# Performance work log

Hardware: AMD Instinct MI355X
Metric: run time of the kernel (lower is better)

Reference implementation:

```python
import jax, jax.numpy as jnp
import numpy as np

NUM_HEADS = 16


def setup_inputs() -> dict:
    key = jax.random.key(0)
    ks = jax.random.split(key, 7)
    B, N, D = 16, 512, 1024
    return {
        "x": jax.random.normal(ks[0], (B, N, D), dtype=jnp.float32),
        "spatial_encoding": jax.random.normal(ks[1], (B, N, N), dtype=jnp.float32),
        "edge_encoding": jax.random.normal(ks[2], (B, N, N), dtype=jnp.float32),
        "Wq": jax.random.normal(ks[3], (D, D), dtype=jnp.float32) * (D ** -0.5),
        "Wk": jax.random.normal(ks[4], (D, D), dtype=jnp.float32) * (D ** -0.5),
        "Wv": jax.random.normal(ks[5], (D, D), dtype=jnp.float32) * (D ** -0.5),
        "Wo": jax.random.normal(ks[6], (D, D), dtype=jnp.float32) * (D ** -0.5),
    }


def reference(x, spatial_encoding, edge_encoding, Wq, Wk, Wv, Wo):
    B, N, D = x.shape
    H = NUM_HEADS
    hd = D // H
    scale = D ** -0.5  # NOTE: source scales by hidden_dim**-0.5, not head_size**-0.5

    def split_heads(t):  # (B,N,D) -> (B,H,N,hd)
        return t.reshape(B, N, H, hd).transpose(0, 2, 1, 3)

    q = split_heads(x @ Wq.T)
    k = split_heads(x @ Wk.T)
    v = split_heads(x @ Wv.T)

    bias = (spatial_encoding + edge_encoding)[:, None]  # (B,1,N,N)
    a = jnp.einsum("bhnd,bhmd->bhnm", q, k) * scale + bias  # (B,H,N,N)

    # rows that are entirely zero (padded) are masked to -inf
    row_nonzero = jnp.any(a != 0, axis=-1, keepdims=True)  # (B,H,N,1)
    a = jnp.where(row_nonzero, a, -jnp.inf)
    p = jax.nn.softmax(a, axis=-1)
    p = jnp.where(jnp.isnan(p), 0.0, p)  # nan_to_num after softmax of all -inf rows

    o = jnp.einsum("bhnm,bhmd->bhnd", p, v)  # (B,H,N,hd)
    o = o.transpose(0, 2, 1, 3).reshape(B, N, D)
    return o @ Wo.T
```

## Files before the change

kernel.cpp:

```cpp
#include <hip/hip_runtime.h>
#include <cstdint>


typedef unsigned short u16;
typedef unsigned int   u32;
typedef __attribute__((ext_vector_type(8))) short bf8;
typedef __attribute__((ext_vector_type(4))) float f4;

__device__ __forceinline__ u16 f2bf(float x) {
  u32 u = __float_as_uint(x);
  u += 0x7FFF + ((u >> 16) & 1);
  return (u16)(u >> 16);
}

__device__ __forceinline__ float bf2f(u16 x) {
  return __uint_as_float(((u32)x) << 16);
}

__device__ __forceinline__ void gl2lds16(const void* g, void* l) {
  __builtin_amdgcn_global_load_lds(
      (const __attribute__((address_space(1))) u32*)g,
      (__attribute__((address_space(3))) u32*)l, 16, 0, 0);
}

__device__ __forceinline__ void barrier_raw() {
  asm volatile("" ::: "memory");
  __builtin_amdgcn_s_barrier();
  asm volatile("" ::: "memory");
}


__global__ __launch_bounds__(256) void cast_bf16(const float* __restrict__ src,
                                                 uint4* __restrict__ dst, int n8) {
  const int i = blockIdx.x * 256 + threadIdx.x;
  if (i >= n8) return;
  const float4* s = (const float4*)src;
  const float4 a = s[2 * i], c = s[2 * i + 1];
  uint4 o;
  o.x = (u32)f2bf(a.x) | ((u32)f2bf(a.y) << 16);
  o.y = (u32)f2bf(a.z) | ((u32)f2bf(a.w) << 16);
  o.z = (u32)f2bf(c.x) | ((u32)f2bf(c.y) << 16);
  o.w = (u32)f2bf(c.z) | ((u32)f2bf(c.w) << 16);
  dst[i] = o;
}

__global__ __launch_bounds__(256) void cast4_bf16(
    const float* __restrict__ s0, const float* __restrict__ s1,
    const float* __restrict__ s2, const float* __restrict__ s3,
    uint4* __restrict__ d0, uint4* __restrict__ d1,
    uint4* __restrict__ d2, uint4* __restrict__ d3) {
  const int i = blockIdx.x * 256 + threadIdx.x;
  const int w = i >> 17, j = i & 131071;
  const float* src = (w == 0) ? s0 : (w == 1) ? s1 : (w == 2) ? s2 : s3;
  uint4* dst = (w == 0) ? d0 : (w == 1) ? d1 : (w == 2) ? d2 : d3;
  const float4* s = (const float4*)src;
  const float4 a = s[2 * j], c = s[2 * j + 1];
  uint4 o;
  o.x = (u32)f2bf(a.x) | ((u32)f2bf(a.y) << 16);
  o.y = (u32)f2bf(a.z) | ((u32)f2bf(a.w) << 16);
  o.z = (u32)f2bf(c.x) | ((u32)f2bf(c.y) << 16);
  o.w = (u32)f2bf(c.z) | ((u32)f2bf(c.w) << 16);
  dst[j] = o;
}

__global__ __launch_bounds__(256) void bias_perm(const float* __restrict__ sp,
                                                 const float* __restrict__ ed,
                                                 u16* __restrict__ Bp) {
  const int jt = blockIdx.x, qt = blockIdx.y, b = blockIdx.z;
  const int tid = threadIdx.x;
  const int wave = tid >> 6, quad = (tid >> 4) & 3, l16 = tid & 15;
  const int qrl = (wave << 4) + (quad << 2);
  union { u16 a[16]; uint4 v[2]; } tmp;
#pragma unroll
  for (int nb = 0; nb < 4; nb++) {
    const int col = (jt << 6) + (nb << 4) + l16;
#pragma unroll
    for (int r = 0; r < 4; r++) {
      const int row = (qt << 6) + qrl + r;
      const size_t idx = ((size_t)b << 18) + (size_t)row * 512 + col;
      tmp.a[nb * 4 + r] = f2bf(sp[idx] + ed[idx]);
    }
  }
  uint4* out = (uint4*)Bp + ((((size_t)b * 8 + qt) * 8 + jt) * 256 + tid) * 2;
  out[0] = tmp.v[0];
  out[1] = tmp.v[1];
}


template <bool SWAP>
__device__ __forceinline__ void gemm_core(const u16* __restrict__ A,
                                          const u16* __restrict__ Bt,
                                          int m0, int n0,
                                          u16* lA, u16* lB, f4 acc[4][4]) {
  const int tid  = threadIdx.x;
  const int wave = tid >> 6;
  const int lane = tid & 63;
  const int quad = lane >> 4;
  const int l16  = lane & 15;
  const int wm   = (wave >> 1) << 6;
  const int wn   = (wave & 1) << 6;
  const int srow = tid >> 3;
  const int scol = ((tid & 7) ^ (srow & 7)) << 3;
  const int c0   = (quad ^ (l16 & 7)) << 3;

  f4 zero = {0.f, 0.f, 0.f, 0.f};
#pragma unroll
  for (int mi = 0; mi < 4; mi++)
#pragma unroll
    for (int ni = 0; ni < 4; ni++) acc[mi][ni] = zero;

  const u16* Ab = A  + (size_t)(m0 + srow) * 1024 + scol;
  const u16* Bb = Bt + (size_t)(n0 + srow) * 1024 + scol;

  for (int k0 = 0; k0 < 1024; k0 += 64) {
    __syncthreads();
#pragma unroll
    for (int i = 0; i < 4; i++) {
      gl2lds16(Ab + (size_t)(i << 5) * 1024 + k0,
               (char*)lA + (((i << 8) + (wave << 6)) << 4));
      gl2lds16(Bb + (size_t)(i << 5) * 1024 + k0,
               (char*)lB + (((i << 8) + (wave << 6)) << 4));
    }
    __syncthreads();
#pragma unroll
    for (int kk = 0; kk < 64; kk += 32) {
      const int o = c0 ^ kk;
      bf8 af[4], bfr[4];
#pragma unroll
      for (int mi = 0; mi < 4; mi++)
        af[mi] = *(const bf8*)(lA + (wm + (mi << 4) + l16) * 64 + o);
#pragma unroll
      for (int ni = 0; ni < 4; ni++)
        bfr[ni] = *(const bf8*)(lB + (wn + (ni << 4) + l16) * 64 + o);
#pragma unroll
      for (int mi = 0; mi < 4; mi++)
#pragma unroll
        for (int ni = 0; ni < 4; ni++) {
          if (SWAP)
            acc[mi][ni] = __builtin_amdgcn_mfma_f32_16x16x32_bf16(
                bfr[ni], af[mi], acc[mi][ni], 0, 0, 0);
          else
            acc[mi][ni] = __builtin_amdgcn_mfma_f32_16x16x32_bf16(
                af[mi], bfr[ni], acc[mi][ni], 0, 0, 0);
        }
    }
  }
}


__global__ __launch_bounds__(256) void qkv_kernel(
    const u16* __restrict__ xb, const u16* __restrict__ wq,
    const u16* __restrict__ wk, const u16* __restrict__ wv,
    u16* __restrict__ Qh, u16* __restrict__ Kh, u16* __restrict__ Vt) {
  __shared__ __align__(16) u16 lA[128 * 64];
  __shared__ __align__(16) u16 lB[128 * 64];
  const int flat = blockIdx.x + (blockIdx.y << 3) + (blockIdx.z << 9);
  const int m_tile = (flat & 7) | (((flat >> 6) & 7) << 3);
  const int n_tile = (flat >> 3) & 7;
  const int proj = flat >> 9;
  const int m0 = m_tile << 7, n0 = n_tile << 7;
  const u16* W = (proj == 0) ? wq : (proj == 1) ? wk : wv;

  const int tid = threadIdx.x, wave = tid >> 6, lane = tid & 63;
  const int quad = lane >> 4, l16 = lane & 15;
  const int wm = (wave >> 1) << 6, wn = (wave & 1) << 6;
  f4 acc[4][4];

  if (proj == 2) {
    gemm_core<false>(xb, W, m0, n0, lA, lB, acc);
#pragma unroll
    for (int mi = 0; mi < 4; mi++) {
      const int gmb = m0 + wm + (mi << 4) + (quad << 2);
      const int b = gmb >> 9, nb = gmb & 511;
#pragma unroll
      for (int ni = 0; ni < 4; ni++) {
        const int gn = n0 + wn + (ni << 4) + l16;
        const int h = gn >> 6, hdi = gn & 63;
        ushort4 pk;
        pk.x = f2bf(acc[mi][ni][0]);
        pk.y = f2bf(acc[mi][ni][1]);
        pk.z = f2bf(acc[mi][ni][2]);
        pk.w = f2bf(acc[mi][ni][3]);
        *(ushort4*)(Vt + ((size_t)((b << 4) + h) * 64 + hdi) * 512 + nb) = pk;
      }
    }
  } else {
    gemm_core<true>(xb, W, m0, n0, lA, lB, acc);
    u16* dst = (proj == 0) ? Qh : Kh;
#pragma unroll
    for (int mi = 0; mi < 4; mi++) {
      const int gm = m0 + wm + (mi << 4) + l16;
      const int b = gm >> 9, n = gm & 511;
#pragma unroll
      for (int ni = 0; ni < 4; ni++) {
        const int gn = n0 + wn + (ni << 4) + (quad << 2);
        const int h = gn >> 6, hdi = gn & 63;
        ushort4 pk;
        pk.x = f2bf(acc[mi][ni][0]);
        pk.y = f2bf(acc[mi][ni][1]);
        pk.z = f2bf(acc[mi][ni][2]);
        pk.w = f2bf(acc[mi][ni][3]);
        *(ushort4*)(dst + ((size_t)((b << 4) + h) * 512 + n) * 64 + hdi) = pk;
      }
    }
  }
}


__global__ __launch_bounds__(256) void oproj_kernel(const u16* __restrict__ Ob,
                                                    const u16* __restrict__ wo,
                                                    float* __restrict__ out) {
  __shared__ __align__(16) u16 lA[128 * 64];
  __shared__ __align__(16) u16 lB[128 * 64];
  const int flat = blockIdx.x + (blockIdx.y << 3);
  const int m0 = ((flat & 7) | (((flat >> 6) & 7) << 3)) << 7;
  const int n0 = ((flat >> 3) & 7) << 7;
  f4 acc[4][4];
  gemm_core<true>(Ob, wo, m0, n0, lA, lB, acc);

  const int tid = threadIdx.x, wave = tid >> 6, lane = tid & 63;
  const int quad = lane >> 4, l16 = lane & 15;
  const int wm = (wave >> 1) << 6, wn = (wave & 1) << 6;
#pragma unroll
  for (int mi = 0; mi < 4; mi++) {
    const int gm = m0 + wm + (mi << 4) + l16;
#pragma unroll
    for (int ni = 0; ni < 4; ni++) {
      const int gn = n0 + wn + (ni << 4) + (quad << 2);
      float4 f;
      f.x = acc[mi][ni][0];
      f.y = acc[mi][ni][1];
      f.z = acc[mi][ni][2];
      f.w = acc[mi][ni][3];
      *(float4*)(out + (size_t)gm * 1024 + gn) = f;
    }
  }
}


__global__ __launch_bounds__(256) void attn_kernel(
    const u16* __restrict__ Qh, const u16* __restrict__ Kh,
    const u16* __restrict__ Vt, const u16* __restrict__ Bp,
    u16* __restrict__ Ob) {
  __shared__ __align__(16) u16 sQ[64 * 64];
  __shared__ __align__(16) u16 sK[2][64 * 64];
  __shared__ __align__(16) u16 sV[2][64 * 64];
  __shared__ __align__(16) u16 sP[4 * 16 * 72];
  const int flat = blockIdx.x + (blockIdx.y << 3) + (blockIdx.z << 7);
  const int qt = (flat >> 3) & 7;
  const int h  = (flat >> 6) & 15;
  const int b  = (flat & 7) | (((flat >> 10) & 1) << 3);
  const int q0 = qt << 6;
  const int tid = threadIdx.x, wave = tid >> 6, lane = tid & 63;
  const int quad = lane >> 4, l16 = lane & 15;
  const int c0  = (quad ^ (l16 & 7)) << 3;
  const int swb = (((tid & 7) ^ ((tid >> 3) & 7)) << 4);

  const u16* Qg = Qh + ((size_t)((b << 4) + h) * 512 + q0) * 64;
  const u16* Kg = Kh + (size_t)((b << 4) + h) * 512 * 64;
  const u16* Vg = Vt + (size_t)((b << 4) + h) * 64 * 512;
  const uint4* Bpg = (const uint4*)Bp + (((size_t)b * 8 + qt) * 8 * 256 + tid) * 2;

#pragma unroll
  for (int i = 0; i < 2; i++) {
    const int e = (i << 8) + tid;
    gl2lds16((const char*)Qg + (e >> 3) * 128 + swb,
             (char*)sQ + (((i << 8) + (wave << 6)) << 4));
  }
#pragma unroll
  for (int i = 0; i < 2; i++) {
    const int e = (i << 8) + tid;
    gl2lds16((const char*)Kg + (e >> 3) * 128 + swb,
             (char*)sK[0] + (((i << 8) + (wave << 6)) << 4));
    gl2lds16((const char*)Vg + (size_t)(e >> 3) * 1024 + swb,
             (char*)sV[0] + (((i << 8) + (wave << 6)) << 4));
  }
  asm volatile("s_waitcnt vmcnt(4)" ::: "memory");
  barrier_raw();

  const bf8 aq0 = *(const bf8*)(sQ + ((wave << 4) + l16) * 64 + c0);
  const bf8 aq1 = *(const bf8*)(sQ + ((wave << 4) + l16) * 64 + (c0 ^ 32));

  f4 o[4];
  f4 zero = {0.f, 0.f, 0.f, 0.f};
#pragma unroll
  for (int i = 0; i < 4; i++) o[i] = zero;
  float lsum[4] = {0.f, 0.f, 0.f, 0.f};
  const int qrl = (wave << 4) + (quad << 2);

  int cur = 0;
  for (int jt = 0; jt < 8; jt++) {
    const uint4 bc0 = Bpg[jt * 512];
    const uint4 bc1 = Bpg[jt * 512 + 1];
    const u32 bw[8] = {bc0.x, bc0.y, bc0.z, bc0.w, bc1.x, bc1.y, bc1.z, bc1.w};

    if (jt < 7) {
      const int j1 = (jt + 1) << 6;
#pragma unroll
      for (int i = 0; i < 2; i++) {
        const int e = (i << 8) + tid;
        gl2lds16((const char*)Kg + (size_t)j1 * 128 + (e >> 3) * 128 + swb,
                 (char*)sK[cur ^ 1] + (((i << 8) + (wave << 6)) << 4));
        gl2lds16((const char*)Vg + (size_t)(e >> 3) * 1024 + j1 * 2 + swb,
                 (char*)sV[cur ^ 1] + (((i << 8) + (wave << 6)) << 4));
      }
      asm volatile("s_waitcnt vmcnt(4)" ::: "memory");
    } else {
      asm volatile("s_waitcnt vmcnt(0)" ::: "memory");
    }
    barrier_raw();

    const u16* kbuf = sK[cur];
    const u16* vbuf = sV[cur];
    u16* pw = sP + wave * (16 * 72);

    __builtin_amdgcn_s_setprio(1);
#pragma unroll
    for (int nb = 0; nb < 4; nb++) {
      bf8 b0 = *(const bf8*)(kbuf + ((nb << 4) + l16) * 64 + c0);
      bf8 b1 = *(const bf8*)(kbuf + ((nb << 4) + l16) * 64 + (c0 ^ 32));
      f4 s = zero;
      s = __builtin_amdgcn_mfma_f32_16x16x32_bf16(aq0, b0, s, 0, 0, 0);
      s = __builtin_amdgcn_mfma_f32_16x16x32_bf16(aq1, b1, s, 0, 0, 0);
#pragma unroll
      for (int r = 0; r < 4; r++) {
        const u32 w = bw[nb * 2 + (r >> 1)];
        const float bias = bf2f((r & 1) ? (u16)(w >> 16) : (u16)(w & 0xFFFF));
        const float ev = __expf(s[r] * 0.03125f + bias);
        lsum[r] += ev;
        pw[((quad << 2) + r) * 72 + (nb << 4) + l16] = f2bf(ev);
      }
    }
    __builtin_amdgcn_s_setprio(0);

    bf8 ap0 = *(const bf8*)(pw + l16 * 72 + (quad << 3));
    bf8 ap1 = *(const bf8*)(pw + l16 * 72 + 32 + (quad << 3));
    __builtin_amdgcn_s_setprio(1);
#pragma unroll
    for (int db = 0; db < 4; db++) {
      bf8 v0 = *(const bf8*)(vbuf + ((db << 4) + l16) * 64 + c0);
      bf8 v1 = *(const bf8*)(vbuf + ((db << 4) + l16) * 64 + (c0 ^ 32));
      o[db] = __builtin_amdgcn_mfma_f32_16x16x32_bf16(ap0, v0, o[db], 0, 0, 0);
      o[db] = __builtin_amdgcn_mfma_f32_16x16x32_bf16(ap1, v1, o[db], 0, 0, 0);
    }
    __builtin_amdgcn_s_setprio(0);

    barrier_raw();
    cur ^= 1;
  }

#pragma unroll
  for (int r = 0; r < 4; r++) {
    float s = lsum[r];
    s += __shfl_xor(s, 1);
    s += __shfl_xor(s, 2);
    s += __shfl_xor(s, 4);
    s += __shfl_xor(s, 8);
    const float inv = 1.f / s;
    const int gr = q0 + qrl + r;
#pragma unroll
    for (int db = 0; db < 4; db++)
      Ob[(size_t)((b << 9) + gr) * 1024 + (h << 6) + (db << 4) + l16] =
          f2bf(o[db][r] * inv);
  }
}


extern "C" void kernel_launch(void* const* d_in, const int* in_sizes, int n_in,
                              void* d_out, int out_size, void* d_ws, size_t ws_size,
                              hipStream_t stream) {
  const float* x  = (const float*)d_in[0];
  const float* sp = (const float*)d_in[1];
  const float* ed = (const float*)d_in[2];
  const float* Wq = (const float*)d_in[3];
  const float* Wk = (const float*)d_in[4];
  const float* Wv = (const float*)d_in[5];
  const float* Wo = (const float*)d_in[6];
  float* out = (float*)d_out;

  char* w = (char*)d_ws;
  u16* xb  = (u16*)(w);
  u16* wqb = (u16*)(w + 16777216);
  u16* wkb = (u16*)(w + 18874368);
  u16* wvb = (u16*)(w + 20971520);
  u16* wob = (u16*)(w + 23068672);
  u16* Qh  = (u16*)(w + 25165824);
  u16* Kh  = (u16*)(w + 41943040);
  u16* Vt  = (u16*)(w + 58720256);
  u16* Ob  = (u16*)(w + 75497472);
  u16* Bp  = (u16*)(w + 92274688);

  cast_bf16<<<4096, 256, 0, stream>>>(x, (uint4*)xb, 1048576);
  cast4_bf16<<<2048, 256, 0, stream>>>(Wq, Wk, Wv, Wo,
                                       (uint4*)wqb, (uint4*)wkb,
                                       (uint4*)wvb, (uint4*)wob);
  bias_perm<<<dim3(8, 8, 16), 256, 0, stream>>>(sp, ed, Bp);

  qkv_kernel<<<dim3(8, 64, 3), 256, 0, stream>>>(xb, wqb, wkb, wvb, Qh, Kh, Vt);
  attn_kernel<<<dim3(8, 16, 16), 256, 0, stream>>>(Qh, Kh, Vt, Bp, Ob);
  oproj_kernel<<<dim3(8, 64, 1), 256, 0, stream>>>(Ob, wob, out);
}
```

Before: 264.3 us.

## Shrink attention LDS footprint: reuse K buffer for Q, single-buffer V, swizzle P

```diff
diff --git a/kernel.cpp b/kernel.cpp
--- a/kernel.cpp
+++ b/kernel.cpp
@@ -28,6 +28,8 @@
   __builtin_amdgcn_s_barrier();
   asm volatile("" ::: "memory");
 }
+
+__device__ __forceinline__ void mem_pin() { asm volatile("" ::: "memory"); }
 
 
 __global__ __launch_bounds__(256) void cast_bf16(const float* __restrict__ src,
@@ -242,10 +244,10 @@
     const u16* __restrict__ Qh, const u16* __restrict__ Kh,
     const u16* __restrict__ Vt, const u16* __restrict__ Bp,
     u16* __restrict__ Ob) {
-  __shared__ __align__(16) u16 sQ[64 * 64];
-  __shared__ __align__(16) u16 sK[2][64 * 64];
-  __shared__ __align__(16) u16 sV[2][64 * 64];
-  __shared__ __align__(16) u16 sP[4 * 16 * 72];
+  __shared__ __align__(16) u16 sK0[64 * 64];
+  __shared__ __align__(16) u16 sK1[64 * 64];
+  __shared__ __align__(16) u16 sV[64 * 64];
+  __shared__ __align__(16) u16 sP[4 * 16 * 64];
   const int flat = blockIdx.x + (blockIdx.y << 3) + (blockIdx.z << 7);
   const int qt = (flat >> 3) & 7;
   const int h  = (flat >> 6) & 15;
@@ -265,21 +267,25 @@
   for (int i = 0; i < 2; i++) {
     const int e = (i << 8) + tid;
     gl2lds16((const char*)Qg + (e >> 3) * 128 + swb,
-             (char*)sQ + (((i << 8) + (wave << 6)) << 4));
+             (char*)sK1 + (((i << 8) + (wave << 6)) << 4));
   }
 #pragma unroll
   for (int i = 0; i < 2; i++) {
     const int e = (i << 8) + tid;
     gl2lds16((const char*)Kg + (e >> 3) * 128 + swb,
-             (char*)sK[0] + (((i << 8) + (wave << 6)) << 4));
-    gl2lds16((const char*)Vg + (size_t)(e >> 3) * 1024 + swb,
-             (char*)sV[0] + (((i << 8) + (wave << 6)) << 4));
-  }
+             (char*)sK0 + (((i << 8) + (wave << 6)) << 4));
+  }
+  mem_pin();
+  uint4 cb0 = Bpg[0];
+  uint4 cb1 = Bpg[1];
+  mem_pin();
   asm volatile("s_waitcnt vmcnt(4)" ::: "memory");
   barrier_raw();
 
-  const bf8 aq0 = *(const bf8*)(sQ + ((wave << 4) + l16) * 64 + c0);
-  const bf8 aq1 = *(const bf8*)(sQ + ((wave << 4) + l16) * 64 + (c0 ^ 32));
+  const bf8 aq0 = *(const bf8*)(sK1 + ((wave << 4) + l16) * 64 + c0);
+  const bf8 aq1 = *(const bf8*)(sK1 + ((wave << 4) + l16) * 64 + (c0 ^ 32));
+  asm volatile("s_waitcnt lgkmcnt(0)" ::: "memory");
+  barrier_raw();
 
   f4 o[4];
   f4 zero = {0.f, 0.f, 0.f, 0.f};
@@ -287,38 +293,47 @@
   for (int i = 0; i < 4; i++) o[i] = zero;
   float lsum[4] = {0.f, 0.f, 0.f, 0.f};
   const int qrl = (wave << 4) + (quad << 2);
-
-  int cur = 0;
+  u16* pw = sP + wave * 1024;
+
   for (int jt = 0; jt < 8; jt++) {
-    const uint4 bc0 = Bpg[jt * 512];
-    const uint4 bc1 = Bpg[jt * 512 + 1];
-    const u32 bw[8] = {bc0.x, bc0.y, bc0.z, bc0.w, bc1.x, bc1.y, bc1.z, bc1.w};
-
+    const u16* kcur = (jt & 1) ? sK1 : sK0;
+    u16* knxt = (jt & 1) ? sK0 : sK1;
+
+    uint4 nb0 = cb0, nb1 = cb1;
+    if (jt < 7) {
+      nb0 = Bpg[(jt + 1) * 512];
+      nb1 = Bpg[(jt + 1) * 512 + 1];
+    }
+    mem_pin();
+#pragma unroll
+    for (int i = 0; i < 2; i++) {
+      const int e = (i << 8) + tid;
+      gl2lds16((const char*)Vg + (size_t)(e >> 3) * 1024 + (jt << 6) * 2 + swb,
+               (char*)sV + (((i << 8) + (wave << 6)) << 4));
+    }
     if (jt < 7) {
       const int j1 = (jt + 1) << 6;
 #pragma unroll
       for (int i = 0; i < 2; i++) {
         const int e = (i << 8) + tid;
         gl2lds16((const char*)Kg + (size_t)j1 * 128 + (e >> 3) * 128 + swb,
-                 (char*)sK[cur ^ 1] + (((i << 8) + (wave << 6)) << 4));
-        gl2lds16((const char*)Vg + (size_t)(e >> 3) * 1024 + j1 * 2 + swb,
-                 (char*)sV[cur ^ 1] + (((i << 8) + (wave << 6)) << 4));
+                 (char*)knxt + (((i << 8) + (wave << 6)) << 4));
       }
-      asm volatile("s_waitcnt vmcnt(4)" ::: "memory");
-    } else {
-      asm volatile("s_waitcnt vmcnt(0)" ::: "memory");
-    }
+    }
+    mem_pin();
+    if (jt < 7)
+      asm volatile("s_waitcnt vmcnt(6)" ::: "memory");
+    else
+      asm volatile("s_waitcnt vmcnt(2)" ::: "memory");
     barrier_raw();
 
-    const u16* kbuf = sK[cur];
-    const u16* vbuf = sV[cur];
-    u16* pw = sP + wave * (16 * 72);
+    const u32 bw[8] = {cb0.x, cb0.y, cb0.z, cb0.w, cb1.x, cb1.y, cb1.z, cb1.w};
 
     __builtin_amdgcn_s_setprio(1);
 #pragma unroll
     for (int nb = 0; nb < 4; nb++) {
-      bf8 b0 = *(const bf8*)(kbuf + ((nb << 4) + l16) * 64 + c0);
-      bf8 b1 = *(const bf8*)(kbuf + ((nb << 4) + l16) * 64 + (c0 ^ 32));
+      bf8 b0 = *(const bf8*)(kcur + ((nb << 4) + l16) * 64 + c0);
+      bf8 b1 = *(const bf8*)(kcur + ((nb << 4) + l16) * 64 + (c0 ^ 32));
       f4 s = zero;
       s = __builtin_amdgcn_mfma_f32_16x16x32_bf16(aq0, b0, s, 0, 0, 0);
       s = __builtin_amdgcn_mfma_f32_16x16x32_bf16(aq1, b1, s, 0, 0, 0);
@@ -328,25 +343,34 @@
         const float bias = bf2f((r & 1) ? (u16)(w >> 16) : (u16)(w & 0xFFFF));
         const float ev = __expf(s[r] * 0.03125f + bias);
         lsum[r] += ev;
-        pw[((quad << 2) + r) * 72 + (nb << 4) + l16] = f2bf(ev);
+        const int row = (quad << 2) + r;
+        const int swc = (((nb << 1) + (l16 >> 3)) ^ (row & 7)) << 3;
+        pw[row * 64 + swc + (l16 & 7)] = f2bf(ev);
       }
     }
     __builtin_amdgcn_s_setprio(0);
 
-    bf8 ap0 = *(const bf8*)(pw + l16 * 72 + (quad << 3));
-    bf8 ap1 = *(const bf8*)(pw + l16 * 72 + 32 + (quad << 3));
+    if (jt < 7)
+      asm volatile("s_waitcnt vmcnt(2)" ::: "memory");
+    else
+      asm volatile("s_waitcnt vmcnt(0)" ::: "memory");
+    barrier_raw();
+
+    bf8 ap0 = *(const bf8*)(pw + l16 * 64 + c0);
+    bf8 ap1 = *(const bf8*)(pw + l16 * 64 + (c0 ^ 32));
     __builtin_amdgcn_s_setprio(1);
 #pragma unroll
     for (int db = 0; db < 4; db++) {
-      bf8 v0 = *(const bf8*)(vbuf + ((db << 4) + l16) * 64 + c0);
-      bf8 v1 = *(const bf8*)(vbuf + ((db << 4) + l16) * 64 + (c0 ^ 32));
+      bf8 v0 = *(const bf8*)(sV + ((db << 4) + l16) * 64 + c0);
+      bf8 v1 = *(const bf8*)(sV + ((db << 4) + l16) * 64 + (c0 ^ 32));
       o[db] = __builtin_amdgcn_mfma_f32_16x16x32_bf16(ap0, v0, o[db], 0, 0, 0);
       o[db] = __builtin_amdgcn_mfma_f32_16x16x32_bf16(ap1, v1, o[db], 0, 0, 0);
     }
     __builtin_amdgcn_s_setprio(0);
 
     barrier_raw();
-    cur ^= 1;
+    cb0 = nb0;
+    cb1 = nb1;
   }
 
 #pragma unroll
```

Result: faster. 254.4 us (-3.7%).
